# Kernel optimization log

Hardware: AMD Instinct MI355X
Metric: run time of the kernel (lower is better)

The kernel has to match this reference:

```python
import jax, jax.numpy as jnp
import numpy as np
import math

B, S, H, NH = 8, 2048, 256, 4
DH = H // NH
EPS = 1e-12


def setup_inputs() -> dict:
    key = jax.random.key(0)
    ks = jax.random.split(key, 20)
    g = lambda k, shape: (jax.random.normal(k, shape, jnp.float32) * 0.02)
    inp = {
        "hidden": jax.random.normal(ks[0], (B, S, H), jnp.float32),
        "Wq": g(ks[1], (H, H)), "bq": jnp.zeros((H,), jnp.float32),
        "Wk": g(ks[2], (H, H)), "bk": jnp.zeros((H,), jnp.float32),
        "Wv": g(ks[3], (H, H)), "bv": jnp.zeros((H,), jnp.float32),
        "Wo": g(ks[4], (H, H)), "bo": jnp.zeros((H,), jnp.float32),
        "W1": g(ks[5], (4 * H, H)), "b1": jnp.zeros((4 * H,), jnp.float32),
        "W2": g(ks[6], (H, 4 * H)), "b2": jnp.zeros((H,), jnp.float32),
        "ln1_w": jnp.ones((H,), jnp.float32), "ln1_b": jnp.zeros((H,), jnp.float32),
        "ln2_w": jnp.ones((H,), jnp.float32), "ln2_b": jnp.zeros((H,), jnp.float32),
        "mask": jax.random.randint(ks[7], (B, S), 0, 2, jnp.int32),
    }
    return inp


def _layernorm(x, w, b):
    u = x.mean(-1, keepdims=True)
    s = ((x - u) ** 2).mean(-1, keepdims=True)
    return w * (x - u) / jnp.sqrt(s + EPS) + b


def _gelu_tanh(h):
    return 0.5 * h * (1.0 + jnp.tanh(math.sqrt(2.0 / math.pi) * (h + 0.044715 * h ** 3)))


def _block(hidden, mask, Wq, bq, Wk, bk, Wv, bv, Wo, bo, W1, b1, W2, b2,
           ln1_w, ln1_b, ln2_w, ln2_b):
    # --- attention sublayer (pre-norm + residual) ---
    x = _layernorm(hidden, ln1_w, ln1_b)
    def heads(W, b):  # [B,S,H] -> [B,NH,S,DH]
        return (x @ W.T + b).reshape(B, S, NH, DH).transpose(0, 2, 1, 3)
    q, k, v = heads(Wq, bq), heads(Wk, bk), heads(Wv, bv)
    corr = jnp.einsum("bhqd,bhkd->bhqk", q, k) / math.sqrt(DH)
    # torch code masks QUERY rows: mask [B,S] broadcast over heads and keys
    corr = jnp.where(mask[:, None, :, None] == 0, -1e9, corr)
    prob = jax.nn.softmax(corr, axis=-1)
    attn = jnp.einsum("bhqk,bhkd->bhqd", prob, v)
    attn = attn.transpose(0, 2, 1, 3).reshape(B, S, H) @ Wo.T + bo
    hidden = hidden + attn
    # --- FFN sublayer (pre-norm + residual) ---
    y = _layernorm(hidden, ln2_w, ln2_b)
    h1 = y @ W1.T + b1
    ff = _gelu_tanh(h1) @ W2.T + b2
    return hidden + ff


def reference(hidden, Wq, bq, Wk, bk, Wv, bv, Wo, bo, W1, b1, W2, b2,
              ln1_w, ln1_b, ln2_w, ln2_b, mask):
    return _block(hidden, mask, Wq, bq, Wk, bk, Wv, bv, Wo, bo,
                  W1, b1, W2, b2, ln1_w, ln1_b, ln2_w, ln2_b)
```

## Files before the change

### kernel.cpp

```cpp
#include <hip/hip_runtime.h>
#include <hip/hip_bf16.h>
#include <cstdint>
#include <cstddef>

constexpr int CB  = 8;
constexpr int CS  = 2048;
constexpr int CH  = 256;
constexpr int CNH = 4;
constexpr int CDH = 64;
constexpr int CT  = CB * CS;

typedef __attribute__((ext_vector_type(8)))  __bf16 bf16x8;
typedef __attribute__((ext_vector_type(4)))  float  f32x4;
typedef __attribute__((ext_vector_type(16))) float  f32x16;
typedef __attribute__((ext_vector_type(2)))  int    i32x2;

__device__ __forceinline__ float b2f(unsigned short u) {
    union { float f; unsigned int i; } v; v.i = ((unsigned int)u) << 16; return v.f;
}
__device__ __forceinline__ unsigned short f2b(float f) {
    union { float f; unsigned int i; } v; v.f = f;
    unsigned int r = v.i + 0x7FFFu + ((v.i >> 16) & 1u);
    return (unsigned short)(r >> 16);
}
__device__ __forceinline__ unsigned short f2b_fast(float f) {
    union { float f; unsigned int i; } v; v.f = f;
    return (unsigned short)((v.i + 0x8000u) >> 16);
}
__device__ __forceinline__ unsigned int packbf(float a, float b) {
    return (unsigned int)f2b_fast(a) | ((unsigned int)f2b_fast(b) << 16);
}
__device__ __forceinline__ float fexp2(float x) {
#if __has_builtin(__builtin_amdgcn_exp2f)
    return __builtin_amdgcn_exp2f(x);
#else
    float r; asm("v_exp_f32 %0, %1" : "=v"(r) : "v"(x)); return r;
#endif
}
__device__ __forceinline__ f32x4 mfma16(bf16x8 a, bf16x8 b, f32x4 c) {
    return __builtin_amdgcn_mfma_f32_16x16x32_bf16(a, b, c, 0, 0, 0);
}
__device__ __forceinline__ f32x16 mfma32(bf16x8 a, bf16x8 b, f32x16 c) {
    return __builtin_amdgcn_mfma_f32_32x32x16_bf16(a, b, c, 0, 0, 0);
}
__device__ __forceinline__ f32x16 zero16() {
    f32x16 z;
    #pragma unroll
    for (int i = 0; i < 16; ++i) z[i] = 0.f;
    return z;
}

#define GLOAD_LDS16(gptr, lptr)                                                        \
    __builtin_amdgcn_global_load_lds((const __attribute__((address_space(1))) void*)(gptr), \
                                     (__attribute__((address_space(3))) void*)(lptr), 16, 0, 0)

#define QSCALE 0.1803368801111204f

__global__ __launch_bounds__(256) void detect_kernel(
    const unsigned short* __restrict__ h, int* __restrict__ flag)
{
    __shared__ int s_bad;
    const int tid = threadIdx.x;
    if (tid == 0) s_bad = 0;
    __syncthreads();
    bool bad = false;
    for (int i = tid; i < 2048; i += 256) {
        float v = b2f(h[i]);
        if (!(fabsf(v) < 1e25f)) bad = true;
    }
    if (bad) s_bad = 1;
    __syncthreads();
    if (tid == 0) *flag = s_bad;
}

struct CvtArgs6  { const void* src[6];  void* dst[6];  int n[6]; };
struct CvtArgs11 { const void* src[11]; void* dst[11]; int n[11]; };

__global__ __launch_bounds__(256) void cvt_to_bf16_k(const int* __restrict__ flag, CvtArgs6 a)
{
    const int seg = blockIdx.y, n = a.n[seg];
    const bool inf32 = (*flag != 0);
    const float* sf = (const float*)a.src[seg];
    const unsigned short* sb = (const unsigned short*)a.src[seg];
    unsigned short* d = (unsigned short*)a.dst[seg];
    for (int i = (blockIdx.x * 256 + threadIdx.x) * 4; i < n; i += gridDim.x * 1024) {
        ushort4 o;
        if (inf32) {
            float4 v = *(const float4*)(sf + i);
            o.x = f2b(v.x); o.y = f2b(v.y); o.z = f2b(v.z); o.w = f2b(v.w);
        } else {
            o = *(const ushort4*)(sb + i);
        }
        *(ushort4*)(d + i) = o;
    }
}

__global__ __launch_bounds__(256) void cvt_to_f32_k(const int* __restrict__ flag, CvtArgs11 a)
{
    const int seg = blockIdx.y, n = a.n[seg];
    const bool inf32 = (*flag != 0);
    const float* sf = (const float*)a.src[seg];
    const unsigned short* sb = (const unsigned short*)a.src[seg];
    float* d = (float*)a.dst[seg];
    for (int i = (blockIdx.x * 256 + threadIdx.x) * 4; i < n; i += gridDim.x * 1024) {
        float4 o;
        if (inf32) {
            o = *(const float4*)(sf + i);
        } else {
            ushort4 v = *(const ushort4*)(sb + i);
            o.x = b2f(v.x); o.y = b2f(v.y); o.z = b2f(v.z); o.w = b2f(v.w);
        }
        *(float4*)(d + i) = o;
    }
}

__global__ __launch_bounds__(256) void ln_kernel(
    const float* __restrict__ x, const float* __restrict__ w,
    const float* __restrict__ b, unsigned short* __restrict__ out)
{
    const int wave = threadIdx.x >> 6, lane = threadIdx.x & 63;
    const int token = blockIdx.x * 4 + wave;
    const int c = lane * 4;
    const size_t rowo = (size_t)token * CH + c;
    float4 u = *(const float4*)(x + rowo);
    float v0 = u.x, v1 = u.y, v2 = u.z, v3 = u.w;
    float s = v0 + v1 + v2 + v3;
    float q = v0*v0 + v1*v1 + v2*v2 + v3*v3;
    #pragma unroll
    for (int m = 1; m < 64; m <<= 1) { s += __shfl_xor(s, m, 64); q += __shfl_xor(q, m, 64); }
    float mean = s * (1.0f/256.0f);
    float var  = q * (1.0f/256.0f) - mean*mean;
    float inv  = rsqrtf(var + 1e-12f);
    float4 ww = *(const float4*)(w + c);
    float4 bb = *(const float4*)(b + c);
    ushort4 o;
    o.x = f2b(ww.x * (v0-mean)*inv + bb.x);
    o.y = f2b(ww.y * (v1-mean)*inv + bb.y);
    o.z = f2b(ww.z * (v2-mean)*inv + bb.z);
    o.w = f2b(ww.w * (v3-mean)*inv + bb.w);
    *(ushort4*)(out + rowo) = o;
}

template<bool GELU, bool RESID, bool HEADSTORE, bool OUTF32, bool OUTDYN>
__device__ __forceinline__ void gemm_core(
    const unsigned short* __restrict__ A, const unsigned short* __restrict__ W,
    const float* __restrict__ bias, const float* __restrict__ resid,
    void* __restrict__ out, const int* __restrict__ flag,
    int K, int N, int m0, int n0, float oscale)
{
    __shared__ __align__(16) unsigned short lA[128*32];
    __shared__ __align__(16) unsigned short lB[128*32];
    const int tid  = threadIdx.x;
    const int lane = tid & 63;
    const int wave = tid >> 6;
    const int wr = (wave >> 1) * 64;
    const int wc = (wave & 1) * 64;
    const int g = lane >> 4, r16 = lane & 15;
    const int lrow = lane >> 2;
    const int lch  = lane & 3;

    const f32x4 zero = {0.f, 0.f, 0.f, 0.f};
    f32x4 acc[4][4];
    #pragma unroll
    for (int m = 0; m < 4; ++m)
        #pragma unroll
        for (int n = 0; n < 4; ++n) acc[m][n] = zero;

    for (int k0 = 0; k0 < K; k0 += 32) {
        #pragma unroll
        for (int i = 0; i < 2; ++i) {
            int chunk = wave + i * 4;
            int row = chunk * 16 + lrow;
            const unsigned short* ga = A + (size_t)(m0 + row) * K + k0 + lch * 8;
            GLOAD_LDS16(ga, &lA[chunk * 512]);
            const unsigned short* gw = W + (size_t)(n0 + row) * K + k0 + lch * 8;
            GLOAD_LDS16(gw, &lB[chunk * 512]);
        }
        __syncthreads();
        bf16x8 af[4], wf[4];
        #pragma unroll
        for (int m = 0; m < 4; ++m) af[m] = *(const bf16x8*)&lA[(wr + m*16 + r16) * 32 + g * 8];
        #pragma unroll
        for (int n = 0; n < 4; ++n) wf[n] = *(const bf16x8*)&lB[(wc + n*16 + r16) * 32 + g * 8];
        #pragma unroll
        for (int m = 0; m < 4; ++m)
            #pragma unroll
            for (int n = 0; n < 4; ++n)
                acc[m][n] = mfma16(af[m], wf[n], acc[m][n]);
        __syncthreads();
    }

    const bool of32dyn = OUTDYN ? (*flag != 0) : false;
    #pragma unroll
    for (int n = 0; n < 4; ++n) {
        int col = n0 + wc + n*16 + r16;
        float bv = bias[col];
        #pragma unroll
        for (int m = 0; m < 4; ++m) {
            int row0 = m0 + wr + m*16 + g*4;
            #pragma unroll
            for (int r = 0; r < 4; ++r) {
                int row = row0 + r;
                float v = (acc[m][n][r] + bv) * oscale;
                if (GELU) {
                    float a = 0.79788456080286541f * (v + 0.044715f * v * v * v);
                    v = v * (1.0f / (1.0f + __expf(-2.0f * a)));
                }
                if (RESID) v += resid[(size_t)row * N + col];
                size_t oidx;
                if (HEADSTORE) {
                    int hh = col >> 6, d = col & 63;
                    int bb = row >> 11, ss = row & 2047;
                    oidx = ((((size_t)bb * CNH + hh) * CS) + ss) * CDH + d;
                } else {
                    oidx = (size_t)row * N + col;
                }
                if (OUTF32)      ((float*)out)[oidx] = v;
                else if (OUTDYN) {
                    if (of32dyn) ((float*)out)[oidx] = v;
                    else         ((unsigned short*)out)[oidx] = f2b(v);
                }
                else             ((unsigned short*)out)[oidx] = f2b(v);
            }
        }
    }
}

__global__ __launch_bounds__(256) void k_qkv(
    const unsigned short* __restrict__ xhat,
    const unsigned short* Wq, const float* bq, unsigned short* q,
    const unsigned short* Wk, const float* bk, unsigned short* k,
    const unsigned short* Wv, const float* bv, unsigned short* v)
{
    const unsigned short* W  = blockIdx.z == 0 ? Wq : (blockIdx.z == 1 ? Wk : Wv);
    const float*          bi = blockIdx.z == 0 ? bq : (blockIdx.z == 1 ? bk : bv);
    unsigned short*       o  = blockIdx.z == 0 ? q  : (blockIdx.z == 1 ? k  : v);
    const float osc = blockIdx.z == 0 ? QSCALE : 1.0f;
    gemm_core<false, false, true, false, false>(xhat, W, bi, nullptr, o, nullptr,
                                                CH, CH, blockIdx.x * 128, blockIdx.y * 128, osc);
}

__global__ __launch_bounds__(256) void k_oproj(
    const unsigned short* __restrict__ A, const unsigned short* __restrict__ W,
    const float* __restrict__ bias, const float* __restrict__ resid,
    float* __restrict__ out)
{
    gemm_core<false, true, false, true, false>(A, W, bias, resid, out, nullptr,
                                               CH, CH, blockIdx.x * 128, blockIdx.y * 128, 1.0f);
}

__global__ __launch_bounds__(256) void k_ffn1(
    const unsigned short* __restrict__ A, const unsigned short* __restrict__ W,
    const float* __restrict__ bias, unsigned short* __restrict__ out)
{
    gemm_core<true, false, false, false, false>(A, W, bias, nullptr, out, nullptr,
                                                CH, 4*CH, blockIdx.x * 128, blockIdx.y * 128, 1.0f);
}

__global__ __launch_bounds__(256) void k_ffn2(
    const unsigned short* __restrict__ A, const unsigned short* __restrict__ W,
    const float* __restrict__ bias, const float* __restrict__ resid,
    void* __restrict__ out, const int* __restrict__ flag)
{
    gemm_core<false, true, false, false, true>(A, W, bias, resid, out, flag,
                                               4*CH, CH, blockIdx.x * 128, blockIdx.y * 128, 1.0f);
}

__global__ __launch_bounds__(256) void vtrans_kernel(
    const unsigned short* __restrict__ v, unsigned short* __restrict__ vt)
{
    __shared__ unsigned short T[64 * 72];
    const int bh = blockIdx.y, s0 = blockIdx.x * 64, tid = threadIdx.x;
    const size_t ibase = (size_t)bh * CS * CDH;
    const size_t obase = (size_t)bh * CDH * CS;
    #pragma unroll
    for (int i = 0; i < 2; ++i) {
        int t2 = tid + i * 256;
        int row = t2 >> 3, ch = t2 & 7;
        uint4 dv = *(const uint4*)(v + ibase + (size_t)(s0 + row) * CDH + ch * 8);
        *(uint4*)&T[row * 72 + ch * 8] = dv;
    }
    __syncthreads();
    #pragma unroll
    for (int i = 0; i < 2; ++i) {
        int t2 = tid + i * 256;
        int d = t2 >> 3, ch = t2 & 7;
        unsigned short tmp[8];
        #pragma unroll
        for (int j = 0; j < 8; ++j) tmp[j] = T[(ch * 8 + j) * 72 + d];
        *(uint4*)(vt + obase + (size_t)d * CS + s0 + ch * 8) = *(uint4*)tmp;
    }
}

__global__ __launch_bounds__(512, 4) void attn_kernel(
    const unsigned short* __restrict__ Q, const unsigned short* __restrict__ Kp,
    const unsigned short* __restrict__ Vt, const int* __restrict__ mask,
    unsigned short* __restrict__ out)
{
    __shared__ __align__(16) char lds[65536];

    const int tid = threadIdx.x, lane = tid & 63, wave = tid >> 6;
    const int qb = wave >> 1, kh = wave & 1;
    const int r32 = lane & 31, hi = lane >> 5;
    const int bh = blockIdx.y, bb = bh >> 2, hh = bh & 3;
    const int q0 = blockIdx.x * 128;
    const size_t baseQ = (size_t)bh * CS * CDH;
    const size_t baseT = (size_t)bh * CDH * CS;

    const int qrow = q0 + qb * 32 + r32;
    bf16x8 qf[4];
    {
        const bool live = (mask[bb * CS + qrow] != 0);
        #pragma unroll
        for (int dw = 0; dw < 4; ++dw) {
            uint4 v = {0u, 0u, 0u, 0u};
            if (live) v = *(const uint4*)(Q + baseQ + (size_t)qrow * CDH + dw * 16 + hi * 8);
            qf[dw] = *(bf16x8*)&v;
        }
    }

#define STAGE(BUF, KT) do {                                                             \
        _Pragma("unroll")                                                               \
        for (int i = 0; i < 2; ++i) {                                                   \
            const int slot0 = i * 512 + wave * 64;                                      \
            const int slot  = slot0 + lane;                                             \
            const int kw = slot >> 7, kk2 = slot & 127;                                 \
            GLOAD_LDS16(Kp + baseQ + (size_t)((KT) + kk2) * CDH + kw * 8,               \
                        lds + (BUF) * 16384 + slot0 * 16);                              \
            const int vc = slot >> 6, vd = slot & 63;                                   \
            GLOAD_LDS16(Vt + baseT + (size_t)vd * CS + (KT) + vc * 8,                   \
                        lds + 32768 + (BUF) * 16384 + slot0 * 16);                      \
        } } while (0)

    f32x16 o0 = zero16(), o1 = zero16();
    float psum = 0.f;

    STAGE(0, 0);
    __syncthreads();

    for (int t = 0; t < CS / 128; ++t) {
        const int buf = t & 1;
        const int kt = t * 128;
        if (t + 1 < CS / 128) STAGE(buf ^ 1, kt + 128);

        const char* kbase = lds + buf * 16384;
        const char* vbase = lds + 32768 + buf * 16384;

        f32x16 sT0 = zero16(), sT1 = zero16();
        __builtin_amdgcn_s_setprio(1);
        #pragma unroll
        for (int dw = 0; dw < 4; ++dw) {
            const char* cb = kbase + (dw * 2 + hi) * 2048;
            bf16x8 k0 = *(const bf16x8*)(cb + (kh * 64 + r32) * 16);
            bf16x8 k1 = *(const bf16x8*)(cb + (kh * 64 + 32 + r32) * 16);
            sT0 = mfma32(k0, qf[dw], sT0);
            sT1 = mfma32(k1, qf[dw], sT1);
        }
        __builtin_amdgcn_s_setprio(0);

#define PROCKB(SREG, KB) do {                                                           \
            float p[16];                                                                \
            _Pragma("unroll")                                                           \
            for (int r = 0; r < 16; ++r) { p[r] = fexp2((SREG)[r]); psum += p[r]; }     \
            _Pragma("unroll")                                                           \
            for (int w = 0; w < 2; ++w) {                                               \
                unsigned int a01 = packbf(p[w*8+0], p[w*8+1]);                          \
                unsigned int a23 = packbf(p[w*8+2], p[w*8+3]);                          \
                unsigned int b01 = packbf(p[w*8+4], p[w*8+5]);                          \
                unsigned int b23 = packbf(p[w*8+6], p[w*8+7]);                          \
                unsigned int ap0, ap1, ap2, ap3;                                        \
                {                                                                       \
                    i32x2 s1 = __builtin_amdgcn_permlane32_swap((int)a01, (int)b01, false, false); \
                    i32x2 s2 = __builtin_amdgcn_permlane32_swap((int)a23, (int)b23, false, false); \
                    ap0 = (unsigned int)s1.x; ap2 = (unsigned int)s1.y;                 \
                    ap1 = (unsigned int)s2.x; ap3 = (unsigned int)s2.y;                 \
                }                                                                       \
                union { unsigned int u[4]; bf16x8 v; } apv;                             \
                apv.u[0] = ap0; apv.u[1] = ap1; apv.u[2] = ap2; apv.u[3] = ap3;         \
                const char* vb2 = vbase + ((kh * 4 + (KB) * 2 + w) * 2 + hi) * 1024;    \
                bf16x8 v0 = *(const bf16x8*)(vb2 + r32 * 16);                           \
                bf16x8 v1 = *(const bf16x8*)(vb2 + (32 + r32) * 16);                    \
                o0 = mfma32(apv.v, v0, o0);                                             \
                o1 = mfma32(apv.v, v1, o1);                                             \
            } } while (0)

        PROCKB(sT0, 0);
        PROCKB(sT1, 1);
#undef PROCKB

        __syncthreads();
    }

    float ps = psum + __shfl_xor(psum, 32, 64);
    float* lsum = (float*)(lds + 32768);
    float* Oex  = (float*)lds;
    if (lane < 32) lsum[(qb * 2 + kh) * 32 + r32] = ps;
    if (kh == 1) {
        #pragma unroll
        for (int r = 0; r < 16; ++r) {
            const int qr = (r & 3) + 8 * (r >> 2) + 4 * hi;
            Oex[(qb * 32 + qr) * 64 + r32]      = o0[r];
            Oex[(qb * 32 + qr) * 64 + 32 + r32] = o1[r];
        }
    }
    __syncthreads();
    if (kh == 0) {
        #pragma unroll
        for (int r = 0; r < 16; ++r) {
            const int qr = (r & 3) + 8 * (r >> 2) + 4 * hi;
            const float l = lsum[(qb * 2 + 0) * 32 + qr] + lsum[(qb * 2 + 1) * 32 + qr];
            const float inv = 1.0f / l;
            const float u0 = (o0[r] + Oex[(qb * 32 + qr) * 64 + r32]) * inv;
            const float u1 = (o1[r] + Oex[(qb * 32 + qr) * 64 + 32 + r32]) * inv;
            const size_t ob = (size_t)(bb * CS + q0 + qb * 32 + qr) * CH + hh * CDH;
            out[ob + r32]      = f2b(u0);
            out[ob + 32 + r32] = f2b(u1);
        }
    }
#undef STAGE
}

extern "C" void kernel_launch(void* const* d_in, const int* in_sizes, int n_in,
                              void* d_out, int out_size, void* d_ws, size_t ws_size,
                              hipStream_t stream)
{
    const void* hidden = d_in[0];
    const void* Wq = d_in[1];  const void* bq = d_in[2];
    const void* Wk = d_in[3];  const void* bk = d_in[4];
    const void* Wv = d_in[5];  const void* bv = d_in[6];
    const void* Wo = d_in[7];  const void* bo = d_in[8];
    const void* W1 = d_in[9];  const void* b1 = d_in[10];
    const void* W2 = d_in[11]; const void* b2 = d_in[12];
    const void* ln1w = d_in[13]; const void* ln1b = d_in[14];
    const void* ln2w = d_in[15]; const void* ln2b = d_in[16];
    const int* mask = (const int*)d_in[17];

    char* ws = (char*)d_ws;
    const size_t KB = 1u << 10, MB = 1u << 20;
    int*            flag  = (int*)ws;
    float*          bqf   = (float*)(ws + 4*KB);
    float*          bkf   = (float*)(ws + 8*KB);
    float*          bvf   = (float*)(ws + 12*KB);
    float*          bof   = (float*)(ws + 16*KB);
    float*          b1f   = (float*)(ws + 20*KB);
    float*          b2f_  = (float*)(ws + 28*KB);
    float*          ln1wf = (float*)(ws + 32*KB);
    float*          ln1bf = (float*)(ws + 36*KB);
    float*          ln2wf = (float*)(ws + 40*KB);
    float*          ln2bf = (float*)(ws + 44*KB);
    unsigned short* Wqb   = (unsigned short*)(ws + 1*MB);
    unsigned short* Wkb   = (unsigned short*)(ws + 1*MB + 256*KB);
    unsigned short* Wvb   = (unsigned short*)(ws + 1*MB + 512*KB);
    unsigned short* Wob   = (unsigned short*)(ws + 1*MB + 768*KB);
    unsigned short* W1b   = (unsigned short*)(ws + 2*MB);
    unsigned short* W2b   = (unsigned short*)(ws + 2*MB + 512*KB);
    float*          hf32  = (float*)(ws + 3*MB);
    unsigned short* xhat  = (unsigned short*)(ws + 19*MB);
    unsigned short* qb    = (unsigned short*)(ws + 27*MB);
    unsigned short* kb    = (unsigned short*)(ws + 35*MB);
    unsigned short* vb    = (unsigned short*)(ws + 43*MB);
    unsigned short* attnb = xhat;
    float*          hid2f = (float*)(ws + 35*MB);
    unsigned short* vtb   = (unsigned short*)(ws + 51*MB);
    unsigned short* yhat  = qb;
    unsigned short* h1g   = (unsigned short*)(ws + 51*MB);

    dim3 blk(256);
    detect_kernel<<<1, blk, 0, stream>>>((const unsigned short*)hidden, flag);

    CvtArgs6 cw;
    cw.src[0]=Wq;  cw.dst[0]=Wqb; cw.n[0]=CH*CH;
    cw.src[1]=Wk;  cw.dst[1]=Wkb; cw.n[1]=CH*CH;
    cw.src[2]=Wv;  cw.dst[2]=Wvb; cw.n[2]=CH*CH;
    cw.src[3]=Wo;  cw.dst[3]=Wob; cw.n[3]=CH*CH;
    cw.src[4]=W1;  cw.dst[4]=W1b; cw.n[4]=4*CH*CH;
    cw.src[5]=W2;  cw.dst[5]=W2b; cw.n[5]=4*CH*CH;
    cvt_to_bf16_k<<<dim3(64, 6), blk, 0, stream>>>(flag, cw);

    CvtArgs11 cf;
    cf.src[0]=hidden; cf.dst[0]=hf32;  cf.n[0]=CT*CH;
    cf.src[1]=bq;     cf.dst[1]=bqf;   cf.n[1]=CH;
    cf.src[2]=bk;     cf.dst[2]=bkf;   cf.n[2]=CH;
    cf.src[3]=bv;     cf.dst[3]=bvf;   cf.n[3]=CH;
    cf.src[4]=bo;     cf.dst[4]=bof;   cf.n[4]=CH;
    cf.src[5]=b1;     cf.dst[5]=b1f;   cf.n[5]=4*CH;
    cf.src[6]=b2;     cf.dst[6]=b2f_;  cf.n[6]=CH;
    cf.src[7]=ln1w;   cf.dst[7]=ln1wf; cf.n[7]=CH;
    cf.src[8]=ln1b;   cf.dst[8]=ln1bf; cf.n[8]=CH;
    cf.src[9]=ln2w;   cf.dst[9]=ln2wf; cf.n[9]=CH;
    cf.src[10]=ln2b;  cf.dst[10]=ln2bf;cf.n[10]=CH;
    cvt_to_f32_k<<<dim3(512, 11), blk, 0, stream>>>(flag, cf);

    ln_kernel<<<CT / 4, blk, 0, stream>>>(hf32, ln1wf, ln1bf, xhat);
    k_qkv<<<dim3(CT / 128, CH / 128, 3), blk, 0, stream>>>(xhat, Wqb, bqf, qb,
                                                           Wkb, bkf, kb, Wvb, bvf, vb);
    vtrans_kernel<<<dim3(CS / 64, CB * CNH), blk, 0, stream>>>(vb, vtb);
    attn_kernel<<<dim3(CS / 128, CB * CNH), dim3(512), 0, stream>>>(qb, kb, vtb, mask, attnb);
    k_oproj<<<dim3(CT / 128, CH / 128), blk, 0, stream>>>(attnb, Wob, bof, hf32, hid2f);
    ln_kernel<<<CT / 4, blk, 0, stream>>>(hid2f, ln2wf, ln2bf, yhat);
    k_ffn1<<<dim3(CT / 128, (4 * CH) / 128), blk, 0, stream>>>(yhat, W1b, b1f, h1g);
    k_ffn2<<<dim3(CT / 128, CH / 128), blk, 0, stream>>>(h1g, W2b, b2f_, hid2f,
                                                         d_out, flag);
}
```

Measured before the change: 167.8 us.

## Store residual stream in bf16, deepen GEMM K-tile, add LDS-staged vectorized epilogue

```diff
diff --git a/kernel.cpp b/kernel.cpp
--- a/kernel.cpp
+++ b/kernel.cpp
@@ -73,10 +73,10 @@
     if (tid == 0) *flag = s_bad;
 }
 
-struct CvtArgs6  { const void* src[6];  void* dst[6];  int n[6]; };
-struct CvtArgs11 { const void* src[11]; void* dst[11]; int n[11]; };
-
-__global__ __launch_bounds__(256) void cvt_to_bf16_k(const int* __restrict__ flag, CvtArgs6 a)
+struct CvtW { const void* src[7]; void* dst[7]; int n[7]; };
+struct CvtB { const void* src[10]; void* dst[10]; int n[10]; };
+
+__global__ __launch_bounds__(256) void cvt_wb_k(const int* __restrict__ flag, CvtW a)
 {
     const int seg = blockIdx.y, n = a.n[seg];
     const bool inf32 = (*flag != 0);
@@ -95,14 +95,15 @@
     }
 }
 
-__global__ __launch_bounds__(256) void cvt_to_f32_k(const int* __restrict__ flag, CvtArgs11 a)
+__global__ __launch_bounds__(256) void cvt_bf_k(const int* __restrict__ flag, CvtB a)
 {
     const int seg = blockIdx.y, n = a.n[seg];
     const bool inf32 = (*flag != 0);
     const float* sf = (const float*)a.src[seg];
     const unsigned short* sb = (const unsigned short*)a.src[seg];
     float* d = (float*)a.dst[seg];
-    for (int i = (blockIdx.x * 256 + threadIdx.x) * 4; i < n; i += gridDim.x * 1024) {
+    const int i = threadIdx.x * 4;
+    if (i < n) {
         float4 o;
         if (inf32) {
             o = *(const float4*)(sf + i);
@@ -115,15 +116,15 @@
 }
 
 __global__ __launch_bounds__(256) void ln_kernel(
-    const float* __restrict__ x, const float* __restrict__ w,
+    const unsigned short* __restrict__ x, const float* __restrict__ w,
     const float* __restrict__ b, unsigned short* __restrict__ out)
 {
     const int wave = threadIdx.x >> 6, lane = threadIdx.x & 63;
     const int token = blockIdx.x * 4 + wave;
     const int c = lane * 4;
     const size_t rowo = (size_t)token * CH + c;
-    float4 u = *(const float4*)(x + rowo);
-    float v0 = u.x, v1 = u.y, v2 = u.z, v3 = u.w;
+    ushort4 u = *(const ushort4*)(x + rowo);
+    float v0 = b2f(u.x), v1 = b2f(u.y), v2 = b2f(u.z), v3 = b2f(u.w);
     float s = v0 + v1 + v2 + v3;
     float q = v0*v0 + v1*v1 + v2*v2 + v3*v3;
     #pragma unroll
@@ -141,23 +142,35 @@
     *(ushort4*)(out + rowo) = o;
 }
 
-template<bool GELU, bool RESID, bool HEADSTORE, bool OUTF32, bool OUTDYN>
+template<bool GELU, bool RESID, bool HEADSTORE, bool OUTDYN>
 __device__ __forceinline__ void gemm_core(
     const unsigned short* __restrict__ A, const unsigned short* __restrict__ W,
-    const float* __restrict__ bias, const float* __restrict__ resid,
+    const float* __restrict__ bias, const unsigned short* __restrict__ resid,
     void* __restrict__ out, const int* __restrict__ flag,
     int K, int N, int m0, int n0, float oscale)
 {
-    __shared__ __align__(16) unsigned short lA[128*32];
-    __shared__ __align__(16) unsigned short lB[128*32];
+    __shared__ __align__(16) char smem[32768];
+    char* lAc = smem;
+    char* lBc = smem + 16384;
+
     const int tid  = threadIdx.x;
     const int lane = tid & 63;
     const int wave = tid >> 6;
     const int wr = (wave >> 1) * 64;
     const int wc = (wave & 1) * 64;
     const int g = lane >> 4, r16 = lane & 15;
-    const int lrow = lane >> 2;
-    const int lch  = lane & 3;
+
+#define GSTAGE(K0) do {                                                                 \
+        _Pragma("unroll")                                                               \
+        for (int j = 0; j < 4; ++j) {                                                   \
+            const int sb_ = j * 256 + wave * 64;                                        \
+            const int kw_ = sb_ >> 7;                                                   \
+            const int r0_ = sb_ & 127;                                                  \
+            GLOAD_LDS16(A + (size_t)(m0 + r0_ + lane) * K + (K0) + kw_ * 8,             \
+                        lAc + sb_ * 16);                                                \
+            GLOAD_LDS16(W + (size_t)(n0 + r0_ + lane) * K + (K0) + kw_ * 8,             \
+                        lBc + sb_ * 16);                                                \
+        } } while (0)
 
     const f32x4 zero = {0.f, 0.f, 0.f, 0.f};
     f32x4 acc[4][4];
@@ -166,63 +179,112 @@
         #pragma unroll
         for (int n = 0; n < 4; ++n) acc[m][n] = zero;
 
-    for (int k0 = 0; k0 < K; k0 += 32) {
-        #pragma unroll
-        for (int i = 0; i < 2; ++i) {
-            int chunk = wave + i * 4;
-            int row = chunk * 16 + lrow;
-            const unsigned short* ga = A + (size_t)(m0 + row) * K + k0 + lch * 8;
-            GLOAD_LDS16(ga, &lA[chunk * 512]);
-            const unsigned short* gw = W + (size_t)(n0 + row) * K + k0 + lch * 8;
-            GLOAD_LDS16(gw, &lB[chunk * 512]);
-        }
+    GSTAGE(0);
+    for (int k0 = 0; k0 < K; k0 += 64) {
         __syncthreads();
-        bf16x8 af[4], wf[4];
-        #pragma unroll
-        for (int m = 0; m < 4; ++m) af[m] = *(const bf16x8*)&lA[(wr + m*16 + r16) * 32 + g * 8];
-        #pragma unroll
-        for (int n = 0; n < 4; ++n) wf[n] = *(const bf16x8*)&lB[(wc + n*16 + r16) * 32 + g * 8];
-        #pragma unroll
-        for (int m = 0; m < 4; ++m)
+        #pragma unroll
+        for (int kk = 0; kk < 2; ++kk) {
+            bf16x8 af[4], wf[4];
+            const int kwb = (kk * 4 + g) * 128;
+            #pragma unroll
+            for (int m = 0; m < 4; ++m)
+                af[m] = *(const bf16x8*)(lAc + (kwb + wr + m*16 + r16) * 16);
             #pragma unroll
             for (int n = 0; n < 4; ++n)
-                acc[m][n] = mfma16(af[m], wf[n], acc[m][n]);
+                wf[n] = *(const bf16x8*)(lBc + (kwb + wc + n*16 + r16) * 16);
+            #pragma unroll
+            for (int m = 0; m < 4; ++m)
+                #pragma unroll
+                for (int n = 0; n < 4; ++n)
+                    acc[m][n] = mfma16(af[m], wf[n], acc[m][n]);
+        }
         __syncthreads();
-    }
-
+        if (k0 + 64 < K) GSTAGE(k0 + 64);
+    }
+#undef GSTAGE
+
+    float* eps = (float*)smem;
+    const int erow = tid >> 2;
+    const int ecb  = (tid & 3) * 32;
     const bool of32dyn = OUTDYN ? (*flag != 0) : false;
+
     #pragma unroll
-    for (int n = 0; n < 4; ++n) {
-        int col = n0 + wc + n*16 + r16;
-        float bv = bias[col];
-        #pragma unroll
-        for (int m = 0; m < 4; ++m) {
-            int row0 = m0 + wr + m*16 + g*4;
-            #pragma unroll
-            for (int r = 0; r < 4; ++r) {
-                int row = row0 + r;
-                float v = (acc[m][n][r] + bv) * oscale;
-                if (GELU) {
-                    float a = 0.79788456080286541f * (v + 0.044715f * v * v * v);
-                    v = v * (1.0f / (1.0f + __expf(-2.0f * a)));
-                }
-                if (RESID) v += resid[(size_t)row * N + col];
-                size_t oidx;
-                if (HEADSTORE) {
-                    int hh = col >> 6, d = col & 63;
-                    int bb = row >> 11, ss = row & 2047;
-                    oidx = ((((size_t)bb * CNH + hh) * CS) + ss) * CDH + d;
-                } else {
-                    oidx = (size_t)row * N + col;
-                }
-                if (OUTF32)      ((float*)out)[oidx] = v;
-                else if (OUTDYN) {
-                    if (of32dyn) ((float*)out)[oidx] = v;
-                    else         ((unsigned short*)out)[oidx] = f2b(v);
-                }
-                else             ((unsigned short*)out)[oidx] = f2b(v);
+    for (int phase = 0; phase < 2; ++phase) {
+        if (phase) __syncthreads();
+        if ((wave >> 1) == phase) {
+            #pragma unroll
+            for (int m = 0; m < 4; ++m)
+                #pragma unroll
+                for (int n = 0; n < 4; ++n)
+                    #pragma unroll
+                    for (int r = 0; r < 4; ++r) {
+                        const int lr = m*16 + g*4 + r;
+                        const int lc = wc + n*16 + r16;
+                        eps[lr * 128 + (lc ^ ((lr & 7) << 2))] = acc[m][n][r];
+                    }
+        }
+        __syncthreads();
+
+        float v[32];
+        const int shift = (erow & 7) << 2;
+        #pragma unroll
+        for (int c = 0; c < 8; ++c)
+            *(f32x4*)&v[c*4] = *(const f32x4*)&eps[erow * 128 + ((ecb + c*4) ^ shift)];
+
+        const int grow = m0 + phase * 64 + erow;
+        const int gcb  = n0 + ecb;
+        float bs[32];
+        #pragma unroll
+        for (int c = 0; c < 8; ++c)
+            *(float4*)&bs[c*4] = *(const float4*)(bias + gcb + c*4);
+        unsigned short rs[32];
+        if (RESID) {
+            #pragma unroll
+            for (int c = 0; c < 4; ++c)
+                *(uint4*)&rs[c*8] = *(const uint4*)(resid + (size_t)grow * N + gcb + c*8);
+        }
+        #pragma unroll
+        for (int c = 0; c < 32; ++c) {
+            float x = (v[c] + bs[c]) * oscale;
+            if (GELU) {
+                float a = 0.79788456080286541f * (x + 0.044715f * x * x * x);
+                x = x * (1.0f / (1.0f + __expf(-2.0f * a)));
             }
-        }
+            if (RESID) x += b2f(rs[c]);
+            v[c] = x;
+        }
+
+        size_t obase;
+        if (HEADSTORE) {
+            const int hh = gcb >> 6, d0 = gcb & 63;
+            const int bb = grow >> 11, ss = grow & 2047;
+            obase = ((((size_t)bb * CNH + hh) * CS) + ss) * CDH + d0;
+        } else {
+            obase = (size_t)grow * N + gcb;
+        }
+        if (OUTDYN && of32dyn) {
+            float* op = (float*)out + obase;
+            #pragma unroll
+            for (int c = 0; c < 8; ++c) *(float4*)(op + c*4) = *(float4*)&v[c*4];
+        } else {
+            unsigned short* op = (unsigned short*)out + obase;
+            #pragma unroll
+            for (int c = 0; c < 4; ++c) {
+                ushort4 pk;
+                pk.x = f2b(v[c*8+0]); pk.y = f2b(v[c*8+1]);
+                pk.z = f2b(v[c*8+2]); pk.w = f2b(v[c*8+3]);
+                ushort4 pk2;
+                pk2.x = f2b(v[c*8+4]); pk2.y = f2b(v[c*8+5]);
+                pk2.z = f2b(v[c*8+6]); pk2.w = f2b(v[c*8+7]);
+                uint4 w16;
+                w16.x = (unsigned int)pk.x  | ((unsigned int)pk.y  << 16);
+                w16.y = (unsigned int)pk.z  | ((unsigned int)pk.w  << 16);
+                w16.z = (unsigned int)pk2.x | ((unsigned int)pk2.y << 16);
+                w16.w = (unsigned int)pk2.z | ((unsigned int)pk2.w << 16);
+                *(uint4*)(op + c*8) = w16;
+            }
+        }
+        if (phase == 0) __syncthreads();
     }
 }
 
@@ -236,34 +298,34 @@
     const float*          bi = blockIdx.z == 0 ? bq : (blockIdx.z == 1 ? bk : bv);
     unsigned short*       o  = blockIdx.z == 0 ? q  : (blockIdx.z == 1 ? k  : v);
     const float osc = blockIdx.z == 0 ? QSCALE : 1.0f;
-    gemm_core<false, false, true, false, false>(xhat, W, bi, nullptr, o, nullptr,
-                                                CH, CH, blockIdx.x * 128, blockIdx.y * 128, osc);
+    gemm_core<false, false, true, false>(xhat, W, bi, nullptr, o, nullptr,
+                                         CH, CH, blockIdx.x * 128, blockIdx.y * 128, osc);
 }
 
 __global__ __launch_bounds__(256) void k_oproj(
     const unsigned short* __restrict__ A, const unsigned short* __restrict__ W,
-    const float* __restrict__ bias, const float* __restrict__ resid,
-    float* __restrict__ out)
-{
-    gemm_core<false, true, false, true, false>(A, W, bias, resid, out, nullptr,
-                                               CH, CH, blockIdx.x * 128, blockIdx.y * 128, 1.0f);
+    const float* __restrict__ bias, const unsigned short* __restrict__ resid,
+    unsigned short* __restrict__ out)
+{
+    gemm_core<false, true, false, false>(A, W, bias, resid, out, nullptr,
+                                         CH, CH, blockIdx.x * 128, blockIdx.y * 128, 1.0f);
 }
 
 __global__ __launch_bounds__(256) void k_ffn1(
     const unsigned short* __restrict__ A, const unsigned short* __restrict__ W,
     const float* __restrict__ bias, unsigned short* __restrict__ out)
 {
-    gemm_core<true, false, false, false, false>(A, W, bias, nullptr, out, nullptr,
-                                                CH, 4*CH, blockIdx.x * 128, blockIdx.y * 128, 1.0f);
+    gemm_core<true, false, false, false>(A, W, bias, nullptr, out, nullptr,
+                                         CH, 4*CH, blockIdx.x * 128, blockIdx.y * 128, 1.0f);
 }
 
 __global__ __launch_bounds__(256) void k_ffn2(
     const unsigned short* __restrict__ A, const unsigned short* __restrict__ W,
-    const float* __restrict__ bias, const float* __restrict__ resid,
+    const float* __restrict__ bias, const unsigned short* __restrict__ resid,
     void* __restrict__ out, const int* __restrict__ flag)
 {
-    gemm_core<false, true, false, false, true>(A, W, bias, resid, out, flag,
-                                               4*CH, CH, blockIdx.x * 128, blockIdx.y * 128, 1.0f);
+    gemm_core<false, true, false, true>(A, W, bias, resid, out, flag,
+                                        4*CH, CH, blockIdx.x * 128, blockIdx.y * 128, 1.0f);
 }
 
 __global__ __launch_bounds__(256) void vtrans_kernel(
@@ -454,51 +516,51 @@
     unsigned short* Wob   = (unsigned short*)(ws + 1*MB + 768*KB);
     unsigned short* W1b   = (unsigned short*)(ws + 2*MB);
     unsigned short* W2b   = (unsigned short*)(ws + 2*MB + 512*KB);
-    float*          hf32  = (float*)(ws + 3*MB);
-    unsigned short* xhat  = (unsigned short*)(ws + 19*MB);
-    unsigned short* qb    = (unsigned short*)(ws + 27*MB);
-    unsigned short* kb    = (unsigned short*)(ws + 35*MB);
-    unsigned short* vb    = (unsigned short*)(ws + 43*MB);
+    unsigned short* hb16  = (unsigned short*)(ws + 3*MB);
+    unsigned short* xhat  = (unsigned short*)(ws + 11*MB);
+    unsigned short* qb    = (unsigned short*)(ws + 19*MB);
+    unsigned short* kb    = (unsigned short*)(ws + 27*MB);
+    unsigned short* vb    = (unsigned short*)(ws + 35*MB);
+    unsigned short* vtb   = (unsigned short*)(ws + 43*MB);
     unsigned short* attnb = xhat;
-    float*          hid2f = (float*)(ws + 35*MB);
-    unsigned short* vtb   = (unsigned short*)(ws + 51*MB);
-    unsigned short* yhat  = qb;
+    unsigned short* hid2b = qb;
+    unsigned short* yhat  = kb;
     unsigned short* h1g   = (unsigned short*)(ws + 51*MB);
 
     dim3 blk(256);
     detect_kernel<<<1, blk, 0, stream>>>((const unsigned short*)hidden, flag);
 
-    CvtArgs6 cw;
-    cw.src[0]=Wq;  cw.dst[0]=Wqb; cw.n[0]=CH*CH;
-    cw.src[1]=Wk;  cw.dst[1]=Wkb; cw.n[1]=CH*CH;
-    cw.src[2]=Wv;  cw.dst[2]=Wvb; cw.n[2]=CH*CH;
-    cw.src[3]=Wo;  cw.dst[3]=Wob; cw.n[3]=CH*CH;
-    cw.src[4]=W1;  cw.dst[4]=W1b; cw.n[4]=4*CH*CH;
-    cw.src[5]=W2;  cw.dst[5]=W2b; cw.n[5]=4*CH*CH;
-    cvt_to_bf16_k<<<dim3(64, 6), blk, 0, stream>>>(flag, cw);
-
-    CvtArgs11 cf;
-    cf.src[0]=hidden; cf.dst[0]=hf32;  cf.n[0]=CT*CH;
-    cf.src[1]=bq;     cf.dst[1]=bqf;   cf.n[1]=CH;
-    cf.src[2]=bk;     cf.dst[2]=bkf;   cf.n[2]=CH;
-    cf.src[3]=bv;     cf.dst[3]=bvf;   cf.n[3]=CH;
-    cf.src[4]=bo;     cf.dst[4]=bof;   cf.n[4]=CH;
-    cf.src[5]=b1;     cf.dst[5]=b1f;   cf.n[5]=4*CH;
-    cf.src[6]=b2;     cf.dst[6]=b2f_;  cf.n[6]=CH;
-    cf.src[7]=ln1w;   cf.dst[7]=ln1wf; cf.n[7]=CH;
-    cf.src[8]=ln1b;   cf.dst[8]=ln1bf; cf.n[8]=CH;
-    cf.src[9]=ln2w;   cf.dst[9]=ln2wf; cf.n[9]=CH;
-    cf.src[10]=ln2b;  cf.dst[10]=ln2bf;cf.n[10]=CH;
-    cvt_to_f32_k<<<dim3(512, 11), blk, 0, stream>>>(flag, cf);
-
-    ln_kernel<<<CT / 4, blk, 0, stream>>>(hf32, ln1wf, ln1bf, xhat);
+    CvtW cw;
+    cw.src[0]=Wq;  cw.dst[0]=Wqb;  cw.n[0]=CH*CH;
+    cw.src[1]=Wk;  cw.dst[1]=Wkb;  cw.n[1]=CH*CH;
+    cw.src[2]=Wv;  cw.dst[2]=Wvb;  cw.n[2]=CH*CH;
+    cw.src[3]=Wo;  cw.dst[3]=Wob;  cw.n[3]=CH*CH;
+    cw.src[4]=W1;  cw.dst[4]=W1b;  cw.n[4]=4*CH*CH;
+    cw.src[5]=W2;  cw.dst[5]=W2b;  cw.n[5]=4*CH*CH;
+    cw.src[6]=hidden; cw.dst[6]=hb16; cw.n[6]=CT*CH;
+    cvt_wb_k<<<dim3(256, 7), blk, 0, stream>>>(flag, cw);
+
+    CvtB cf;
+    cf.src[0]=bq;    cf.dst[0]=bqf;   cf.n[0]=CH;
+    cf.src[1]=bk;    cf.dst[1]=bkf;   cf.n[1]=CH;
+    cf.src[2]=bv;    cf.dst[2]=bvf;   cf.n[2]=CH;
+    cf.src[3]=bo;    cf.dst[3]=bof;   cf.n[3]=CH;
+    cf.src[4]=b1;    cf.dst[4]=b1f;   cf.n[4]=4*CH;
+    cf.src[5]=b2;    cf.dst[5]=b2f_;  cf.n[5]=CH;
+    cf.src[6]=ln1w;  cf.dst[6]=ln1wf; cf.n[6]=CH;
+    cf.src[7]=ln1b;  cf.dst[7]=ln1bf; cf.n[7]=CH;
+    cf.src[8]=ln2w;  cf.dst[8]=ln2wf; cf.n[8]=CH;
+    cf.src[9]=ln2b;  cf.dst[9]=ln2bf; cf.n[9]=CH;
+    cvt_bf_k<<<dim3(1, 10), blk, 0, stream>>>(flag, cf);
+
+    ln_kernel<<<CT / 4, blk, 0, stream>>>(hb16, ln1wf, ln1bf, xhat);
     k_qkv<<<dim3(CT / 128, CH / 128, 3), blk, 0, stream>>>(xhat, Wqb, bqf, qb,
                                                            Wkb, bkf, kb, Wvb, bvf, vb);
     vtrans_kernel<<<dim3(CS / 64, CB * CNH), blk, 0, stream>>>(vb, vtb);
     attn_kernel<<<dim3(CS / 128, CB * CNH), dim3(512), 0, stream>>>(qb, kb, vtb, mask, attnb);
-    k_oproj<<<dim3(CT / 128, CH / 128), blk, 0, stream>>>(attnb, Wob, bof, hf32, hid2f);
-    ln_kernel<<<CT / 4, blk, 0, stream>>>(hid2f, ln2wf, ln2bf, yhat);
+    k_oproj<<<dim3(CT / 128, CH / 128), blk, 0, stream>>>(attnb, Wob, bof, hb16, hid2b);
+    ln_kernel<<<CT / 4, blk, 0, stream>>>(hid2b, ln2wf, ln2bf, yhat);
     k_ffn1<<<dim3(CT / 128, (4 * CH) / 128), blk, 0, stream>>>(yhat, W1b, b1f, h1g);
-    k_ffn2<<<dim3(CT / 128, CH / 128), blk, 0, stream>>>(h1g, W2b, b2f_, hid2f,
+    k_ffn2<<<dim3(CT / 128, CH / 128), blk, 0, stream>>>(h1g, W2b, b2f_, hid2b,
                                                          d_out, flag);
 }
```

Result: slower. 199.3 us (+18.8%).
